# Optimization experiments

Measured on AMD Instinct MI355X. Metric: run time of the kernel, lower is better.

## Reference

```python
import jax, jax.numpy as jnp
import numpy as np

# init config (matches init_kwargs)
NO_TRANS = False
SPATIAL_SCALE = 0.0625
POOLED = 7
SAMPLES = 2          # sampling_ratio (sample_per_part)
TRANS_STD = 0.1

B, C, H, W = 2, 256, 96, 96
N_ROIS = 512


def setup_inputs() -> dict:
    key = jax.random.key(0)
    k1, k2, k3, k4, k5 = jax.random.split(key, 5)
    bottom_data = jax.random.normal(k1, (B, C, H, W), dtype=jnp.float32)
    img = H / SPATIAL_SCALE  # image-space extent (1536)
    bidx = jax.random.randint(k2, (N_ROIS,), 0, B).astype(jnp.float32)
    xy1 = jax.random.uniform(k3, (N_ROIS, 2), minval=0.0, maxval=0.7 * img)
    wh = jax.random.uniform(k4, (N_ROIS, 2), minval=0.05 * img, maxval=0.3 * img)
    bottom_rois = jnp.concatenate([bidx[:, None], xy1, xy1 + wh], axis=1)  # [N,5]
    bottom_trans = jax.random.normal(k5, (N_ROIS, 2, POOLED, POOLED), dtype=jnp.float32)
    return {"bottom_data": bottom_data, "bottom_rois": bottom_rois, "bottom_trans": bottom_trans}


def _deform_psroi_pool(feat, rois, trans):
    # feat [B,C,H,W], rois [N,5], trans [N,2,P,P] -> out [N,C,P,P]
    Hf, Wf = feat.shape[2], feat.shape[3]
    b = rois[:, 0].astype(jnp.int32)                                    # [N]
    # CUDA kernel rounds roi coords, shifts by -0.5
    x1 = jnp.round(rois[:, 1]) * SPATIAL_SCALE - 0.5
    y1 = jnp.round(rois[:, 2]) * SPATIAL_SCALE - 0.5
    x2 = (jnp.round(rois[:, 3]) + 1.0) * SPATIAL_SCALE - 0.5
    y2 = (jnp.round(rois[:, 4]) + 1.0) * SPATIAL_SCALE - 0.5
    rw = jnp.maximum(x2 - x1, 0.1)
    rh = jnp.maximum(y2 - y1, 0.1)
    bin_w = rw / POOLED
    bin_h = rh / POOLED
    sub_w = bin_w / SAMPLES
    sub_h = bin_h / SAMPLES

    grid = jnp.arange(POOLED, dtype=feat.dtype)
    # part_size == pooled_size and group_size == 1 -> part_h=ph, part_w=pw, class 0
    if NO_TRANS:
        trans_x = jnp.zeros((rois.shape[0], POOLED, POOLED), feat.dtype)
        trans_y = trans_x
    else:
        trans_x = trans[:, 0] * TRANS_STD  # [N,P,P]
        trans_y = trans[:, 1] * TRANS_STD

    # bin start coords per (n, ph, pw)
    wstart = grid[None, None, :] * bin_w[:, None, None] + x1[:, None, None] + trans_x * rw[:, None, None]
    hstart = grid[None, :, None] * bin_h[:, None, None] + y1[:, None, None] + trans_y * rh[:, None, None]

    s = jnp.arange(SAMPLES, dtype=feat.dtype)
    # sample coords [N,P,P,S(ih),S(iw)]
    w = wstart[:, :, :, None, None] + s[None, None, None, None, :] * sub_w[:, None, None, None, None]
    h = hstart[:, :, :, None, None] + s[None, None, None, :, None] * sub_h[:, None, None, None, None]

    valid = (w >= -0.5) & (w <= Wf - 0.5) & (h >= -0.5) & (h <= Hf - 0.5)
    wc = jnp.clip(w, 0.0, Wf - 1.0)
    hc = jnp.clip(h, 0.0, Hf - 1.0)
    x0 = jnp.floor(wc); y0 = jnp.floor(hc)
    dx = wc - x0; dy = hc - y0
    x0i = x0.astype(jnp.int32); y0i = y0.astype(jnp.int32)
    x1i = jnp.ceil(wc).astype(jnp.int32); y1i = jnp.ceil(hc).astype(jnp.int32)

    feat_hwc = jnp.transpose(feat, (0, 2, 3, 1))  # [B,H,W,C]
    bb = b[:, None, None, None, None]

    def gather(yi, xi):
        return feat_hwc[bb, yi, xi]  # [N,P,P,S,S,C]

    w00 = ((1.0 - dx) * (1.0 - dy))[..., None]
    w01 = (dx * (1.0 - dy))[..., None]
    w10 = ((1.0 - dx) * dy)[..., None]
    w11 = (dx * dy)[..., None]
    val = (w00 * gather(y0i, x0i) + w01 * gather(y0i, x1i)
           + w10 * gather(y1i, x0i) + w11 * gather(y1i, x1i))
    val = jnp.where(valid[..., None], val, 0.0)

    ssum = val.sum(axis=(3, 4))                              # [N,P,P,C]
    count = valid.astype(feat.dtype).sum(axis=(3, 4))        # [N,P,P]
    out = jnp.where(count[..., None] > 0, ssum / jnp.maximum(count[..., None], 1.0), 0.0)
    return jnp.transpose(out, (0, 3, 1, 2))                  # [N,C,P,P]


def reference(bottom_data, bottom_rois, bottom_trans):
    return _deform_psroi_pool(bottom_data, bottom_rois, bottom_trans)
```

## Files before the change

kernel.cpp:

```cpp
#include <hip/hip_runtime.h>

#define B_      2
#define C_      256
#define H_      96
#define W_      96
#define HW_     (H_ * W_)
#define P_      7
#define PP_     (P_ * P_)
#define NROIS_  512
#define SCALE_  0.0625f
#define TSTD_   0.1f

#define NGROUP_ 8
#define GC_     (C_ / NGROUP_)

typedef float vf4 __attribute__((ext_vector_type(4)));

__device__ __forceinline__ unsigned f2bf(float f) {
    union { float f; unsigned u; } x; x.f = f;
    return (x.u + 0x7fffu + ((x.u >> 16) & 1u)) >> 16;
}
__device__ __forceinline__ float bf_lo(unsigned u) {
    union { unsigned i; float f; } x; x.i = u << 16; return x.f;
}
__device__ __forceinline__ float bf_hi(unsigned u) {
    union { unsigned i; float f; } x; x.i = u & 0xffff0000u; return x.f;
}

__global__ __launch_bounds__(256) void nchw_to_gp_bf16(const float* __restrict__ in,
                                                       ushort* __restrict__ out) {
    __shared__ float tile[32][36];
    const int b   = blockIdx.z;
    const int g   = blockIdx.x & (NGROUP_ - 1);
    const int p0  = (blockIdx.x >> 3) * 32;
    const int c0  = g * 32;
    const int tid = threadIdx.x;

    const float* src = in + (size_t)b * (C_ * HW_);
    ushort*      dst = out + ((size_t)(b * NGROUP_ + g) * HW_) * GC_;

    {
        const int cr = tid >> 3;
        const int pq = (tid & 7) * 4;
        const vf4 v = __builtin_nontemporal_load(
            (const vf4*)&src[(size_t)(c0 + cr) * HW_ + p0 + pq]);
        *(vf4*)&tile[cr][pq] = v;
    }
    __syncthreads();

    {
        const int p  = tid >> 3;
        const int cq = (tid & 7) * 4;
        uint2 o;
        o.x = f2bf(tile[cq + 0][p]) | (f2bf(tile[cq + 1][p]) << 16);
        o.y = f2bf(tile[cq + 2][p]) | (f2bf(tile[cq + 3][p]) << 16);
        *(uint2*)&((unsigned*)dst)[(size_t)(p0 + p) * (GC_ / 2) + (cq >> 1)] = o;
    }
}

__global__ __launch_bounds__(256, 4) void dpsroi_pool7(const ushort* __restrict__ feat,
                                                       const float* __restrict__ rois,
                                                       const float* __restrict__ trans,
                                                       float* __restrict__ out) {
    __shared__ float sout[GC_ * PP_];

    const int blk = blockIdx.x;
    const int g   = blk & (NGROUP_ - 1);
    const int n   = blk >> 3;
    const int tid = threadIdx.x;
    const int bin = tid >> 2;
    const int ch0 = (tid & 3) * 8;

    const int   broi = (int)rois[n * 5 + 0];
    const float x1 = rintf(rois[n * 5 + 1]) * SCALE_ - 0.5f;
    const float y1 = rintf(rois[n * 5 + 2]) * SCALE_ - 0.5f;
    const float x2 = (rintf(rois[n * 5 + 3]) + 1.0f) * SCALE_ - 0.5f;
    const float y2 = (rintf(rois[n * 5 + 4]) + 1.0f) * SCALE_ - 0.5f;
    const float rw = fmaxf(x2 - x1, 0.1f);
    const float rh = fmaxf(y2 - y1, 0.1f);
    const float bin_w = rw * (1.0f / 7.0f);
    const float bin_h = rh * (1.0f / 7.0f);
    const float sub_w = bin_w * 0.5f;
    const float sub_h = bin_h * 0.5f;

    const ushort* fb = feat + ((size_t)(broi * NGROUP_ + g) * HW_) * GC_ + ch0;

    if (bin < PP_) {
        const int pi = bin / P_;
        const int pj = bin - pi * P_;
        const float tx = trans[((n * 2 + 0) * P_ + pi) * P_ + pj] * TSTD_;
        const float ty = trans[((n * 2 + 1) * P_ + pi) * P_ + pj] * TSTD_;
        const float wstart = (float)pj * bin_w + x1 + tx * rw;
        const float hstart = (float)pi * bin_h + y1 + ty * rh;

        float wt[16];
        int   ofs[16];
        int   cnt = 0;
#pragma unroll
        for (int s = 0; s < 4; ++s) {
            const float w = wstart + (float)(s & 1) * sub_w;
            const float h = hstart + (float)(s >> 1) * sub_h;
            const bool valid = (w >= -0.5f) & (w <= (float)W_ - 0.5f) &
                               (h >= -0.5f) & (h <= (float)H_ - 0.5f);
            cnt += valid ? 1 : 0;
            const float vf = valid ? 1.0f : 0.0f;
            const float wc  = fminf(fmaxf(w, 0.0f), (float)(W_ - 1));
            const float hc  = fminf(fmaxf(h, 0.0f), (float)(H_ - 1));
            const float x0f = floorf(wc), y0f = floorf(hc);
            const float dx  = wc - x0f,   dy  = hc - y0f;
            const int   x0  = (int)x0f,   y0  = (int)y0f;
            const int   xp  = (int)ceilf(wc), yp = (int)ceilf(hc);
            wt[4 * s + 0] = vf * (1.0f - dx) * (1.0f - dy);
            wt[4 * s + 1] = vf * dx * (1.0f - dy);
            wt[4 * s + 2] = vf * (1.0f - dx) * dy;
            wt[4 * s + 3] = vf * dx * dy;
            ofs[4 * s + 0] = y0 * W_ + x0;
            ofs[4 * s + 1] = y0 * W_ + xp;
            ofs[4 * s + 2] = yp * W_ + x0;
            ofs[4 * s + 3] = yp * W_ + xp;
        }

        uint4 v[16];
#pragma unroll
        for (int i = 0; i < 16; ++i)
            v[i] = *(const uint4*)(fb + (size_t)ofs[i] * GC_);

        float acc[8] = {0.f, 0.f, 0.f, 0.f, 0.f, 0.f, 0.f, 0.f};
#pragma unroll
        for (int i = 0; i < 16; ++i) {
            const float wgt = wt[i];
            acc[0] += wgt * bf_lo(v[i].x);
            acc[1] += wgt * bf_hi(v[i].x);
            acc[2] += wgt * bf_lo(v[i].y);
            acc[3] += wgt * bf_hi(v[i].y);
            acc[4] += wgt * bf_lo(v[i].z);
            acc[5] += wgt * bf_hi(v[i].z);
            acc[6] += wgt * bf_lo(v[i].w);
            acc[7] += wgt * bf_hi(v[i].w);
        }

        const float inv = (cnt > 0) ? (1.0f / (float)cnt) : 0.0f;
#pragma unroll
        for (int j = 0; j < 8; ++j)
            sout[(ch0 + j) * PP_ + bin] = acc[j] * inv;
    }

    __syncthreads();
    float* outn = out + ((size_t)n * C_ + g * GC_) * PP_;
    for (int f = tid; f < GC_ * PP_; f += 256)
        __builtin_nontemporal_store(sout[f], &outn[f]);
}

extern "C" void kernel_launch(void* const* d_in, const int* in_sizes, int n_in,
                              void* d_out, int out_size, void* d_ws, size_t ws_size,
                              hipStream_t stream) {
    const float* feat  = (const float*)d_in[0];
    const float* rois  = (const float*)d_in[1];
    const float* trans = (const float*)d_in[2];
    float* out = (float*)d_out;

    ushort* gp = (ushort*)d_ws;
    dim3 tb(256);
    dim3 tg((HW_ / 32) * NGROUP_, 1, B_);
    nchw_to_gp_bf16<<<tg, tb, 0, stream>>>(feat, gp);
    dpsroi_pool7<<<NROIS_ * NGROUP_, 256, 0, stream>>>(gp, rois, trans, out);
}
```

Before: 91.11 us.

## Stage ROI bounding-box feature patch in LDS before bilinear sampling

```diff
diff --git a/kernel.cpp b/kernel.cpp
--- a/kernel.cpp
+++ b/kernel.cpp
@@ -14,6 +14,9 @@
 #define NGROUP_ 8
 #define GC_     (C_ / NGROUP_)
 
+#define PATCH_MAX 400
+#define PXSTRIDE  20
+
 typedef float vf4 __attribute__((ext_vector_type(4)));
 
 __device__ __forceinline__ unsigned f2bf(float f) {
@@ -47,7 +50,6 @@
         *(vf4*)&tile[cr][pq] = v;
     }
     __syncthreads();
-
     {
         const int p  = tid >> 3;
         const int cq = (tid & 7) * 4;
@@ -62,14 +64,21 @@
                                                        const float* __restrict__ rois,
                                                        const float* __restrict__ trans,
                                                        float* __restrict__ out) {
+    __shared__ __align__(16) unsigned patch[PATCH_MAX * PXSTRIDE];
     __shared__ float sout[GC_ * PP_];
+    __shared__ float ttab[2 * PP_];
+    __shared__ int   bb[4];
 
     const int blk = blockIdx.x;
     const int g   = blk & (NGROUP_ - 1);
     const int n   = blk >> 3;
     const int tid = threadIdx.x;
     const int bin = tid >> 2;
-    const int ch0 = (tid & 3) * 8;
+    const int chq = tid & 3;
+    const int ch0 = chq * 8;
+
+    if (tid < 2 * PP_) ttab[tid] = trans[n * (2 * PP_) + tid];
+    if (tid == 0) { bb[0] = 1 << 30; bb[1] = -(1 << 30); bb[2] = 1 << 30; bb[3] = -(1 << 30); }
 
     const int   broi = (int)rois[n * 5 + 0];
     const float x1 = rintf(rois[n * 5 + 1]) * SCALE_ - 0.5f;
@@ -83,19 +92,28 @@
     const float sub_w = bin_w * 0.5f;
     const float sub_h = bin_h * 0.5f;
 
-    const ushort* fb = feat + ((size_t)(broi * NGROUP_ + g) * HW_) * GC_ + ch0;
-
+    __syncthreads();
+
+    float wt[16];
+    int   xs0[4], xs1[4], ys0[4], ys1[4];
+    int   cnt = 0;
     if (bin < PP_) {
         const int pi = bin / P_;
         const int pj = bin - pi * P_;
-        const float tx = trans[((n * 2 + 0) * P_ + pi) * P_ + pj] * TSTD_;
-        const float ty = trans[((n * 2 + 1) * P_ + pi) * P_ + pj] * TSTD_;
+        const float tx = ttab[bin] * TSTD_;
+        const float ty = ttab[PP_ + bin] * TSTD_;
         const float wstart = (float)pj * bin_w + x1 + tx * rw;
         const float hstart = (float)pi * bin_h + y1 + ty * rh;
 
-        float wt[16];
-        int   ofs[16];
-        int   cnt = 0;
+        if (chq == 0) {
+            const int xlo = (int)floorf(fminf(fmaxf(wstart, 0.0f), (float)(W_ - 1)));
+            const int xhi = (int)ceilf (fminf(fmaxf(wstart + sub_w, 0.0f), (float)(W_ - 1)));
+            const int ylo = (int)floorf(fminf(fmaxf(hstart, 0.0f), (float)(H_ - 1)));
+            const int yhi = (int)ceilf (fminf(fmaxf(hstart + sub_h, 0.0f), (float)(H_ - 1)));
+            atomicMin(&bb[0], xlo); atomicMax(&bb[1], xhi);
+            atomicMin(&bb[2], ylo); atomicMax(&bb[3], yhi);
+        }
+
 #pragma unroll
         for (int s = 0; s < 4; ++s) {
             const float w = wstart + (float)(s & 1) * sub_w;
@@ -108,37 +126,80 @@
             const float hc  = fminf(fmaxf(h, 0.0f), (float)(H_ - 1));
             const float x0f = floorf(wc), y0f = floorf(hc);
             const float dx  = wc - x0f,   dy  = hc - y0f;
-            const int   x0  = (int)x0f,   y0  = (int)y0f;
-            const int   xp  = (int)ceilf(wc), yp = (int)ceilf(hc);
+            xs0[s] = (int)x0f;           ys0[s] = (int)y0f;
+            xs1[s] = (int)ceilf(wc);     ys1[s] = (int)ceilf(hc);
             wt[4 * s + 0] = vf * (1.0f - dx) * (1.0f - dy);
             wt[4 * s + 1] = vf * dx * (1.0f - dy);
             wt[4 * s + 2] = vf * (1.0f - dx) * dy;
             wt[4 * s + 3] = vf * dx * dy;
-            ofs[4 * s + 0] = y0 * W_ + x0;
-            ofs[4 * s + 1] = y0 * W_ + xp;
-            ofs[4 * s + 2] = yp * W_ + x0;
-            ofs[4 * s + 3] = yp * W_ + xp;
-        }
-
-        uint4 v[16];
-#pragma unroll
-        for (int i = 0; i < 16; ++i)
-            v[i] = *(const uint4*)(fb + (size_t)ofs[i] * GC_);
-
-        float acc[8] = {0.f, 0.f, 0.f, 0.f, 0.f, 0.f, 0.f, 0.f};
-#pragma unroll
-        for (int i = 0; i < 16; ++i) {
-            const float wgt = wt[i];
-            acc[0] += wgt * bf_lo(v[i].x);
-            acc[1] += wgt * bf_hi(v[i].x);
-            acc[2] += wgt * bf_lo(v[i].y);
-            acc[3] += wgt * bf_hi(v[i].y);
-            acc[4] += wgt * bf_lo(v[i].z);
-            acc[5] += wgt * bf_hi(v[i].z);
-            acc[6] += wgt * bf_lo(v[i].w);
-            acc[7] += wgt * bf_hi(v[i].w);
-        }
-
+        }
+    }
+    __syncthreads();
+
+    const int bx0 = bb[0], by0 = bb[2];
+    const int pw  = bb[1] - bb[0] + 1;
+    const int ph  = bb[3] - bb[2] + 1;
+    const int mrows = PATCH_MAX / pw;
+    const int nst   = (ph - 1) / (mrows - 1) + 1;
+
+    int ks[4] = {0, 0, 0, 0};
+    if (bin < PP_) {
+#pragma unroll
+        for (int s = 0; s < 4; ++s) ks[s] = (ys0[s] - by0) / (mrows - 1);
+    }
+
+    const int pw4 = pw * 4;
+    int colpad = 128; while (colpad < pw4) colpad <<= 1;
+    const int csh = __builtin_ctz(colpad);
+
+    const uint4* fb4 = (const uint4*)(feat + ((size_t)(broi * NGROUP_ + g) * HW_) * GC_);
+
+    float acc[8] = {0.f, 0.f, 0.f, 0.f, 0.f, 0.f, 0.f, 0.f};
+
+    for (int k = 0; k < nst; ++k) {
+        const int ys    = by0 + k * (mrows - 1);
+        const int rem   = by0 + ph - ys;
+        const int srows = (mrows < rem) ? mrows : rem;
+
+        for (int t = tid; t < (srows << csh); t += 256) {
+            const int r  = t >> csh;
+            const int c4 = t & (colpad - 1);
+            if (c4 < pw4) {
+                const int px = r * pw + (c4 >> 2);
+                *(uint4*)&patch[px * PXSTRIDE + (c4 & 3) * 4] =
+                    fb4[((size_t)(ys + r) * W_ + bx0) * 4 + c4];
+            }
+        }
+        __syncthreads();
+
+        if (bin < PP_) {
+            const unsigned* pbase = patch + chq * 4;
+#pragma unroll
+            for (int s = 0; s < 4; ++s) {
+                if (ks[s] == k) {
+                    const int ry0 = ys0[s] - ys, ry1 = ys1[s] - ys;
+                    const int cx0 = xs0[s] - bx0, cx1 = xs1[s] - bx0;
+                    const uint4 v00 = *(const uint4*)&pbase[(ry0 * pw + cx0) * PXSTRIDE];
+                    const uint4 v01 = *(const uint4*)&pbase[(ry0 * pw + cx1) * PXSTRIDE];
+                    const uint4 v10 = *(const uint4*)&pbase[(ry1 * pw + cx0) * PXSTRIDE];
+                    const uint4 v11 = *(const uint4*)&pbase[(ry1 * pw + cx1) * PXSTRIDE];
+                    const float w00 = wt[4 * s + 0], w01 = wt[4 * s + 1];
+                    const float w10 = wt[4 * s + 2], w11 = wt[4 * s + 3];
+                    acc[0] += w00 * bf_lo(v00.x) + w01 * bf_lo(v01.x) + w10 * bf_lo(v10.x) + w11 * bf_lo(v11.x);
+                    acc[1] += w00 * bf_hi(v00.x) + w01 * bf_hi(v01.x) + w10 * bf_hi(v10.x) + w11 * bf_hi(v11.x);
+                    acc[2] += w00 * bf_lo(v00.y) + w01 * bf_lo(v01.y) + w10 * bf_lo(v10.y) + w11 * bf_lo(v11.y);
+                    acc[3] += w00 * bf_hi(v00.y) + w01 * bf_hi(v01.y) + w10 * bf_hi(v10.y) + w11 * bf_hi(v11.y);
+                    acc[4] += w00 * bf_lo(v00.z) + w01 * bf_lo(v01.z) + w10 * bf_lo(v10.z) + w11 * bf_lo(v11.z);
+                    acc[5] += w00 * bf_hi(v00.z) + w01 * bf_hi(v01.z) + w10 * bf_hi(v10.z) + w11 * bf_hi(v11.z);
+                    acc[6] += w00 * bf_lo(v00.w) + w01 * bf_lo(v01.w) + w10 * bf_lo(v10.w) + w11 * bf_lo(v11.w);
+                    acc[7] += w00 * bf_hi(v00.w) + w01 * bf_hi(v01.w) + w10 * bf_hi(v10.w) + w11 * bf_hi(v11.w);
+                }
+            }
+        }
+        __syncthreads();
+    }
+
+    if (bin < PP_) {
         const float inv = (cnt > 0) ? (1.0f / (float)cnt) : 0.0f;
 #pragma unroll
         for (int j = 0; j < 8; ++j)
```

After: 127.0 us. 39.4% more time.
